# Kernel optimization log

Measured on AMD Instinct MI355X. Metric: run time of the kernel, lower is better.

The kernel has to match this reference:

```python
import jax, jax.numpy as jnp
import numpy as np
from jax import lax

B, S, E, H, V, L = 16, 256, 256, 256, 50000, 9


def setup_inputs() -> dict:
    key = jax.random.key(0)
    ks = jax.random.split(key, 12)
    s = 0.05
    return {
        "input_ids": jax.random.randint(ks[0], (B, S), 0, V),
        "attention_mask": jnp.ones((B, S), dtype=jnp.int32),
        "labels": jax.random.randint(ks[1], (B, S), 0, L),
        "embedding": jax.random.normal(ks[2], (V, E), jnp.float32) * s,
        "w_ih_l0": jax.random.normal(ks[3], (2, 4 * H, E), jnp.float32) * s,
        "w_ih_rest": jax.random.normal(ks[4], (3, 2, 4 * H, 2 * H), jnp.float32) * s,
        "w_hh": jax.random.normal(ks[5], (4, 2, 4 * H, H), jnp.float32) * s,
        "b": jax.random.normal(ks[6], (4, 2, 2, 4 * H), jnp.float32) * s,
        "ln_g": jnp.ones((2 * H,), jnp.float32),
        "ln_b": jnp.zeros((2 * H,), jnp.float32),
        "lin_w": jax.random.normal(ks[7], (L, 2 * H), jnp.float32) * s,
        "lin_b": jnp.zeros((L,), jnp.float32),
        "crf_start": jax.random.normal(ks[8], (L,), jnp.float32) * s,
        "crf_end": jax.random.normal(ks[9], (L,), jnp.float32) * s,
        "crf_trans": jax.random.normal(ks[10], (L, L), jnp.float32) * s,
    }


def _lstm_dir(x, w_ih, w_hh, b_ih, b_hh, reverse):
    # x: [B,S,in]; PyTorch gate order i,f,g,o packed along 4H.
    Bb = x.shape[0]
    Hh = w_hh.shape[1]
    xg = jnp.einsum('bsi,gi->bsg', x, w_ih) + b_ih + b_hh  # precompute input projection
    if reverse:
        xg = xg[:, ::-1]

    def step(carry, g):
        h, c = carry
        g = g + h @ w_hh.T
        i, f, gg, o = jnp.split(g, 4, axis=-1)
        c = jax.nn.sigmoid(f) * c + jax.nn.sigmoid(i) * jnp.tanh(gg)
        h = jax.nn.sigmoid(o) * jnp.tanh(c)
        return (h, c), h

    z = jnp.zeros((Bb, Hh), x.dtype)
    _, hs = lax.scan(step, (z, z), jnp.swapaxes(xg, 0, 1))
    hs = jnp.swapaxes(hs, 0, 1)  # [B,S,H]
    if reverse:
        hs = hs[:, ::-1]
    return hs


def _forward(input_ids, attention_mask, labels, embedding, w_ih_l0, w_ih_rest,
             w_hh, b, ln_g, ln_b, lin_w, lin_b, crf_start, crf_end, crf_trans):
    x = embedding[input_ids]  # [B,S,E]
    for layer in range(4):
        wf = w_ih_l0[0] if layer == 0 else w_ih_rest[layer - 1, 0]
        wb = w_ih_l0[1] if layer == 0 else w_ih_rest[layer - 1, 1]
        hf = _lstm_dir(x, wf, w_hh[layer, 0], b[layer, 0, 0], b[layer, 0, 1], False)
        hb = _lstm_dir(x, wb, w_hh[layer, 1], b[layer, 1, 0], b[layer, 1, 1], True)
        x = jnp.concatenate([hf, hb], axis=-1)  # [B,S,2H]
    # dropout is identity in eval mode
    mu = x.mean(-1, keepdims=True)
    var = ((x - mu) ** 2).mean(-1, keepdims=True)
    x = (x - mu) * lax.rsqrt(var + 1e-5) * ln_g + ln_b
    logits = jnp.einsum('bsh,lh->bsl', x, lin_w) + lin_b  # emissions [B,S,L]

    # CRF negative log-likelihood (torchcrf semantics, reduction='sum')
    Bb = logits.shape[0]
    mask_f = attention_mask.astype(logits.dtype)
    bidx = jnp.arange(Bb)
    first = labels[:, 0]
    num = crf_start[first] + logits[bidx, 0, first]
    em_t = jnp.swapaxes(logits, 0, 1)[1:]  # [S-1,B,L]
    tprev = labels[:, :-1].T
    tcur = labels[:, 1:].T
    mt = mask_f[:, 1:].T

    def num_step(s, inp):
        e, tp, tc, m = inp
        return s + (crf_trans[tp, tc] + e[bidx, tc]) * m, None

    num, _ = lax.scan(num_step, num, (em_t, tprev, tcur, mt))
    last = jnp.sum(attention_mask, axis=1).astype(jnp.int32) - 1
    num = num + crf_end[labels[bidx, last]]

    alpha = crf_start + logits[:, 0]  # [B,L]

    def den_step(a, inp):
        e, m = inp
        nxt = jax.nn.logsumexp(a[:, :, None] + crf_trans[None] + e[:, None, :], axis=1)
        return jnp.where(m[:, None] > 0, nxt, a), None

    alpha, _ = lax.scan(den_step, alpha, (em_t, mt))
    denom = jax.nn.logsumexp(alpha + crf_end, axis=-1)
    loss = -(num - denom).sum()
    return logits, loss


def reference(input_ids, attention_mask, labels, embedding, w_ih_l0, w_ih_rest,
              w_hh, b, ln_g, ln_b, lin_w, lin_b, crf_start, crf_end, crf_trans):
    return _forward(input_ids, attention_mask, labels, embedding, w_ih_l0,
                    w_ih_rest, w_hh, b, ln_g, ln_b, lin_w, lin_b,
                    crf_start, crf_end, crf_trans)
```

## Files before the change

### kernel.cpp

```cpp
#include <hip/hip_runtime.h>
#include <math.h>
#include <stdint.h>

#define BB 16
#define SS 256
#define LL 9
#define ROWS 4096
#define HP 272

typedef __attribute__((ext_vector_type(8))) short short8;
typedef __attribute__((ext_vector_type(4))) float f32x4;
typedef __attribute__((ext_vector_type(8))) int i32x8;

#define HSCALE 256.0f
#define LOG2E  1.44269504f
#define WCONST 1477.3199f
#define SCALE_ONE 0x7F7F7F7Fu
#define SCALE_IFO 0x6D6D6D6Du
#define SCALE_G   0x6E6E6E6Eu

__device__ __forceinline__ unsigned short f2bf(float f) {
  unsigned u = __float_as_uint(f);
  return (unsigned short)((u + 0x7FFF + ((u >> 16) & 1)) >> 16);
}
__device__ __forceinline__ float bf2f(unsigned short s) {
  return __uint_as_float(((unsigned)s) << 16);
}

__device__ __forceinline__ void gl2lds16(const void* g, void* l) {
  __builtin_amdgcn_global_load_lds(
      (const __attribute__((address_space(1))) void*)g,
      (__attribute__((address_space(3))) void*)l, 16, 0, 0);
}

__global__ __launch_bounds__(256) void embed_bf16(
    const int* __restrict__ ids, const float* __restrict__ emb,
    unsigned short* __restrict__ x0) {
  int row = blockIdx.x;
  int id = ids[row];
  x0[(size_t)row * 256 + threadIdx.x] = f2bf(emb[(size_t)id * 256 + threadIdx.x]);
}

__global__ __launch_bounds__(64) void pack_whh_mx(
    const float* __restrict__ w, unsigned* __restrict__ wfrag) {
  int nb = blockIdx.x, ks2 = blockIdx.y, z = blockIdx.z;
  int lane = threadIdx.x, qq = lane >> 4, col = lane & 15;
  int g = nb >> 4;
  float csc = (g == 2) ? WCONST : -WCONST;
  const float* wp = w + (size_t)z * 1024 * 256 + (size_t)(nb * 16 + col) * 256 +
                    ks2 * 128 + qq * 32;
  unsigned* op = wfrag + (((size_t)(z * 64 + nb) * 2 + ks2) * 64 + lane) * 8;
#pragma unroll
  for (int u = 0; u < 8; ++u) {
    float v0 = wp[u * 4 + 0] * csc, v1 = wp[u * 4 + 1] * csc;
    float v2 = wp[u * 4 + 2] * csc, v3 = wp[u * 4 + 3] * csc;
    unsigned pk = __builtin_amdgcn_cvt_pk_fp8_f32(v0, v1, 0, false);
    pk = __builtin_amdgcn_cvt_pk_fp8_f32(v2, v3, pk, true);
    op[u] = pk;
  }
}

__global__ __launch_bounds__(256) void bias_perm(
    const float* __restrict__ b2, float* __restrict__ biasPF) {
  int i = blockIdx.x * 256 + threadIdx.x;
  int l = i >> 11, r = i & 2047;
  int dir = r >> 10, np = r & 1023;
  int n = ((np & 3) << 8) + (np >> 2);
  float cg = ((np & 3) == 2) ? (2.0f * LOG2E) : (-LOG2E);
  biasPF[i] = (b2[l * 4096 + dir * 2048 + n] + b2[l * 4096 + dir * 2048 + 1024 + n]) * cg;
}

__global__ __launch_bounds__(256) void prep_wih(
    const float* __restrict__ w_l0, const float* __restrict__ w_rest,
    unsigned short* __restrict__ wp, const long* __restrict__ woff_dummy) {
  int l = blockIdx.z;
  int Ksh = l ? 9 : 8;
  int K = 1 << Ksh;
  long total = (long)2 * 1024 * K;
  long idx = (long)blockIdx.x * 256 + threadIdx.x;
  if (idx >= total) return;
  int k = (int)(idx & (K - 1));
  long r = idx >> Ksh;
  int np = (int)(r & 1023), dir = (int)(r >> 10);
  int nph = ((np & 3) << 8) + (np >> 2);
  float cg = ((np & 3) == 2) ? (2.0f * LOG2E) : (-LOG2E);
  const float* src = l ? (w_rest + (size_t)(l - 1) * 2 * 1024 * 512) : w_l0;
  size_t off = l ? (524288 + (size_t)(l - 1) * 1048576) : 0;
  wp[off + idx] = f2bf(src[((size_t)dir * 1024 + nph) * K + k] * cg);
}

__global__ __launch_bounds__(512) void gemm_xg128(
    const unsigned short* __restrict__ A, int K,
    const unsigned short* __restrict__ BP,
    const float* __restrict__ biasPF,
    unsigned short* __restrict__ xgP) {
  int dir = blockIdx.z;
  int n0 = blockIdx.x * 128, m0 = blockIdx.y * 128;
  int tid = threadIdx.x;
  int wv = tid >> 6, lane = tid & 63, quad = lane >> 4, col = lane & 15;
  __shared__ unsigned short As[128 * 32];
  __shared__ unsigned short Bs[128 * 32];
  const unsigned short* Bw = BP + (size_t)dir * 1024 * K;

  int srow = lane >> 2;
  int scol = (lane & 3) * 8;
  const unsigned short* ga = A + (size_t)(m0 + wv * 16 + srow) * K + scol;
  const unsigned short* gb = Bw + (size_t)(n0 + wv * 16 + srow) * K + scol;
  unsigned short* lA = &As[wv * 512];
  unsigned short* lB = &Bs[wv * 512];

  int wm = wv & 1;
  int wn = wv >> 1;
  f32x4 acc[4][2];
#pragma unroll
  for (int mt = 0; mt < 4; ++mt)
#pragma unroll
    for (int nt = 0; nt < 2; ++nt) acc[mt][nt] = (f32x4){0.f, 0.f, 0.f, 0.f};

  for (int k0 = 0; k0 < K; k0 += 32) {
    __syncthreads();
    gl2lds16(ga, lA);
    gl2lds16(gb, lB);
    ga += 32; gb += 32;
    __syncthreads();
    short8 bf0 = *(const short8*)&Bs[(wn * 32 + col) * 32 + quad * 8];
    short8 bf1 = *(const short8*)&Bs[(wn * 32 + 16 + col) * 32 + quad * 8];
#pragma unroll
    for (int mt = 0; mt < 4; ++mt) {
      short8 af = *(const short8*)&As[(wm * 64 + mt * 16 + col) * 32 + quad * 8];
      acc[mt][0] = __builtin_amdgcn_mfma_f32_16x16x32_bf16(af, bf0, acc[mt][0], 0, 0, 0);
      acc[mt][1] = __builtin_amdgcn_mfma_f32_16x16x32_bf16(af, bf1, acc[mt][1], 0, 0, 0);
    }
  }

#pragma unroll
  for (int nt = 0; nt < 2; ++nt) {
    int np = n0 + wn * 32 + nt * 16 + col;
    float bia = biasPF[dir * 1024 + np];
#pragma unroll
    for (int mt = 0; mt < 4; ++mt) {
#pragma unroll
      for (int r = 0; r < 4; ++r) {
        int row = m0 + wm * 64 + mt * 16 + quad * 4 + r;
        xgP[((size_t)dir * ROWS + row) * 1024 + np] = f2bf(acc[mt][nt][r] + bia);
      }
    }
  }
}

__global__ __launch_bounds__(512, 2) void lstm_mx(
    const unsigned short* __restrict__ xgP,
    const unsigned* __restrict__ wfrag,
    unsigned short* __restrict__ xout) {
  int dir = blockIdx.x & 1;
  int bg = blockIdx.x >> 1;
  int tid = threadIdx.x;
  int wv = tid >> 6, lane = tid & 63;
  int quad = lane >> 4, col = lane & 15;

  __shared__ __align__(16) unsigned char Hfrag[2][2 * HP];

  {
    int* hz = (int*)&Hfrag[0][0];
    for (int i = tid; i < HP; i += 512) hz[i] = 0;
  }

  i32x8 wf[2][4][2];
#pragma unroll
  for (int hbi = 0; hbi < 2; ++hbi)
#pragma unroll
    for (int g = 0; g < 4; ++g) {
      int nb = g * 16 + 2 * wv + hbi;
#pragma unroll
      for (int ks2 = 0; ks2 < 2; ++ks2)
        wf[hbi][g][ks2] = *(const i32x8*)(wfrag +
            (((size_t)(dir * 64 + nb) * 2 + ks2) * 64 + lane) * 8);
    }

  int aoff = ((lane & 15) >> 3) * HP + (lane >> 4) * 32;

  int hbsel = quad & 1;
  int bq = quad >> 1;
  int j = 32 * wv + 16 * hbsel + col;
  int b = bg * 2 + bq;
  int pos0 = dir ? (SS - 1) : 0;
  int dstep = dir ? -1 : 1;
  const unsigned short* xq_ptr =
      xgP + ((size_t)dir * ROWS + (size_t)b * SS + pos0) * 1024 + j * 4;
  unsigned short* xo_ptr = xout + ((size_t)b * SS + pos0) * 512 + dir * 256 + j;
  int xq_d = dstep * 1024;
  int xo_d = dstep * 512;
  int hw = bq * HP + j;

  float Cp = 0.f;
  unsigned short ph = 0;
  unsigned short* xo_prev = xo_ptr;
  int cur = 0;
  __syncthreads();

  for (int t = 0; t < SS; ++t) {
    if (t) *xo_prev = ph;
    ushort4 xq = *(const ushort4*)xq_ptr;
    xq_ptr += xq_d;

    i32x8 af0 = *(const i32x8*)&Hfrag[cur][aoff];
    i32x8 af1 = *(const i32x8*)&Hfrag[cur][aoff + 128];
    f32x4 acc[2][4];
#pragma unroll
    for (int hbi = 0; hbi < 2; ++hbi) {
#pragma unroll
      for (int g = 0; g < 4; ++g) {
        f32x4 a = (f32x4){0.f, 0.f, 0.f, 0.f};
        a = __builtin_amdgcn_mfma_scale_f32_16x16x128_f8f6f4(
                af0, wf[hbi][g][0], a, 0, 0, 0, SCALE_ONE, 0,
                (g == 2) ? SCALE_G : SCALE_IFO);
        a = __builtin_amdgcn_mfma_scale_f32_16x16x128_f8f6f4(
                af1, wf[hbi][g][1], a, 0, 0, 0, SCALE_ONE, 0,
                (g == 2) ? SCALE_G : SCALE_IFO);
        acc[hbi][g] = a;
      }
    }

    int nxt = cur ^ 1;
    float a_i = hbsel ? acc[1][0][0] : acc[0][0][0];
    float a_f = hbsel ? acc[1][1][0] : acc[0][1][0];
    float a_g = hbsel ? acc[1][2][0] : acc[0][2][0];
    float a_o = hbsel ? acc[1][3][0] : acc[0][3][0];
    float gi = a_i + bf2f(xq.x);
    float gf = a_f + bf2f(xq.y);
    float gt = a_g + bf2f(xq.z);
    float go = a_o + bf2f(xq.w);
    float si = __builtin_amdgcn_rcpf(1.0f + __builtin_amdgcn_exp2f(gi));
    float sf = __builtin_amdgcn_rcpf(1.0f + __builtin_amdgcn_exp2f(gf));
    float so = __builtin_amdgcn_rcpf(1.0f + __builtin_amdgcn_exp2f(go));
    float rg = __builtin_amdgcn_rcpf(1.0f + __builtin_amdgcn_exp2f(gt));
    float tg2 = fmaf(-4.0f * LOG2E, rg, 2.0f * LOG2E);
    Cp = fmaf(sf, Cp, si * tg2);
    float rc = __builtin_amdgcn_rcpf(1.0f + __builtin_amdgcn_exp2f(Cp));
    float h = so * fmaf(-2.0f, rc, 1.0f);
    unsigned pk = __builtin_amdgcn_cvt_pk_fp8_f32(h * HSCALE, h * HSCALE, 0, false);
    Hfrag[nxt][hw] = (unsigned char)(pk & 0xFF);
    ph = f2bf(h);
    xo_prev = xo_ptr;
    xo_ptr += xo_d;
    __syncthreads();
    cur = nxt;
  }
  *xo_prev = ph;
}

__global__ __launch_bounds__(64) void ln_logits(
    const unsigned short* __restrict__ X, const float* __restrict__ g,
    const float* __restrict__ bt, const float* __restrict__ W,
    const float* __restrict__ lb, float* __restrict__ out) {
  int row = blockIdx.x;
  int lane = threadIdx.x;
  const unsigned short* x = X + (size_t)row * 512;
  float v[8];
  float s = 0.f, s2 = 0.f;
#pragma unroll
  for (int i = 0; i < 8; ++i) {
    v[i] = bf2f(x[lane + 64 * i]);
    s += v[i];
    s2 += v[i] * v[i];
  }
#pragma unroll
  for (int off = 32; off; off >>= 1) {
    s += __shfl_down(s, off, 64);
    s2 += __shfl_down(s2, off, 64);
  }
  s = __shfl(s, 0, 64);
  s2 = __shfl(s2, 0, 64);
  float mu = s * (1.f / 512.f);
  float var = s2 * (1.f / 512.f) - mu * mu;
  float rstd = rsqrtf(var + 1e-5f);
  float y[8];
#pragma unroll
  for (int i = 0; i < 8; ++i) {
    int e = lane + 64 * i;
    y[i] = (v[i] - mu) * rstd * g[e] + bt[e];
  }
  for (int l = 0; l < LL; ++l) {
    float p = 0.f;
#pragma unroll
    for (int i = 0; i < 8; ++i) p += y[i] * W[(size_t)l * 512 + lane + 64 * i];
#pragma unroll
    for (int off = 32; off; off >>= 1) p += __shfl_down(p, off, 64);
    if (lane == 0) out[(size_t)row * LL + l] = p + lb[l];
  }
}

__global__ __launch_bounds__(256) void crf_kernel(
    const float* __restrict__ logits, const int* __restrict__ labels,
    const int* __restrict__ mask, const float* __restrict__ cs,
    const float* __restrict__ ce, const float* __restrict__ ct,
    float* __restrict__ loss_out) {
  __shared__ float trans[9][12];
  __shared__ float alpha[2][BB][12];
  __shared__ float numsh[BB];
  __shared__ float res[BB];
  int tid = threadIdx.x;
  int b = tid >> 4;
  int i = tid & 15;
  if (tid < 81) trans[tid / 9][tid % 9] = ct[tid];
  __syncthreads();
  const float* lg = logits + (size_t)b * SS * LL;
  const int* lbp = labels + (size_t)b * SS;
  const int* mk = mask + (size_t)b * SS;

  float np = 0.f;
  int msum = 0;
  for (int t = i; t < SS; t += 16) {
    msum += mk[t];
    if (t == 0) {
      int l0 = lbp[0];
      np += cs[l0] + lg[l0];
    } else {
      float m = (float)mk[t];
      np += (trans[lbp[t - 1]][lbp[t]] + lg[(size_t)t * LL + lbp[t]]) * m;
    }
  }
#pragma unroll
  for (int off = 8; off; off >>= 1) {
    np += __shfl_down(np, off, 16);
    msum += __shfl_down(msum, off, 16);
  }
  if (i == 0) {
    int last = msum - 1;
    numsh[b] = np + ce[lbp[last]];
  }

  if (i < LL) alpha[0][b][i] = cs[i] + lg[i];
  int cur = 0;
  for (int t = 1; t < SS; ++t) {
    if (i < LL) {
      float e = lg[(size_t)t * LL + i];
      float av[9];
      float mmax = -1e30f;
#pragma unroll
      for (int p = 0; p < LL; ++p) {
        float vv = alpha[cur][b][p] + trans[p][i];
        av[p] = vv;
        mmax = fmaxf(mmax, vv);
      }
      float ssum = 0.f;
#pragma unroll
      for (int p = 0; p < LL; ++p) ssum += __expf(av[p] - mmax);
      float anew = e + mmax + logf(ssum);
      float aold = alpha[cur][b][i];
      alpha[cur ^ 1][b][i] = (mk[t] > 0) ? anew : aold;
    }
    cur ^= 1;
  }
  if (i == 0) {
    float arr[9];
    float m2 = -1e30f;
#pragma unroll
    for (int cc = 0; cc < LL; ++cc) {
      arr[cc] = alpha[cur][b][cc] + ce[cc];
      m2 = fmaxf(m2, arr[cc]);
    }
    float ssd = 0.f;
#pragma unroll
    for (int cc = 0; cc < LL; ++cc) ssd += __expf(arr[cc] - m2);
    float denom = m2 + logf(ssd);
    res[b] = numsh[b] - denom;
  }
  __syncthreads();
  if (tid == 0) {
    float Lsum = 0.f;
    for (int b2 = 0; b2 < BB; ++b2) Lsum += res[b2];
    loss_out[0] = -Lsum;
  }
}

extern "C" void kernel_launch(void* const* d_in, const int* in_sizes, int n_in,
                              void* d_out, int out_size, void* d_ws, size_t ws_size,
                              hipStream_t stream) {
  const int* input_ids = (const int*)d_in[0];
  const int* attn_mask = (const int*)d_in[1];
  const int* labels = (const int*)d_in[2];
  const float* embedding = (const float*)d_in[3];
  const float* w_ih_l0 = (const float*)d_in[4];
  const float* w_ih_rest = (const float*)d_in[5];
  const float* w_hh = (const float*)d_in[6];
  const float* bvec = (const float*)d_in[7];
  const float* ln_g = (const float*)d_in[8];
  const float* ln_b = (const float*)d_in[9];
  const float* lin_w = (const float*)d_in[10];
  const float* lin_b = (const float*)d_in[11];
  const float* crf_start = (const float*)d_in[12];
  const float* crf_end = (const float*)d_in[13];
  const float* crf_trans = (const float*)d_in[14];
  float* out = (float*)d_out;
  char* base = (char*)d_ws;

  unsigned short* x0    = (unsigned short*)(base);
  unsigned short* xoutA = (unsigned short*)(base + (2u << 20));
  unsigned short* xoutB = (unsigned short*)(base + (6u << 20));
  unsigned short* xgP   = (unsigned short*)(base + (10u << 20));
  unsigned*       wfrag = (unsigned*)(base + (26u << 20));
  float*          biasPF= (float*)(base + (28u << 20));
  unsigned short* wihP  = (unsigned short*)(base + (29u << 20));

  embed_bf16<<<ROWS, 256, 0, stream>>>(input_ids, embedding, x0);
  pack_whh_mx<<<dim3(64, 2, 8), 64, 0, stream>>>(w_hh, wfrag);
  bias_perm<<<32, 256, 0, stream>>>(bvec, biasPF);
  prep_wih<<<dim3(4096, 1, 4), 256, 0, stream>>>(w_ih_l0, w_ih_rest, wihP, nullptr);

  const size_t WOFF[4] = {0, 524288, 1572864, 2621440};

  const unsigned short* cur = x0;
  unsigned short* nxt = xoutA;
  for (int l = 0; l < 4; ++l) {
    int K = l ? 512 : 256;
    gemm_xg128<<<dim3(8, 32, 2), 512, 0, stream>>>(
        cur, K, wihP + WOFF[l], biasPF + (size_t)l * 2048, xgP);
    lstm_mx<<<16, 512, 0, stream>>>(xgP, wfrag + (size_t)l * 131072, nxt);
    cur = nxt;
    nxt = (nxt == xoutA) ? xoutB : xoutA;
  }

  ln_logits<<<ROWS, 64, 0, stream>>>(cur, ln_g, ln_b, lin_w, lin_b, out);
  crf_kernel<<<1, 256, 0, stream>>>(out, labels, attn_mask, crf_start, crf_end,
                                    crf_trans, out + (size_t)ROWS * LL);
}
```

Measured before the change: 1.200 ms.

## Restructure LSTM recurrence to 1024-thread blocks covering four batch rows each

The recurrent kernel now runs 8 blocks of 16 waves, with each wave owning 16 hidden units across four batch rows, in place of 16 blocks of 8 waves handling two rows. Each wave now issues half as many MFMAs per step and holds half the weight fragments in registers. The input-projection gates are fed in as the MFMA accumulator seed and are prefetched one step ahead, and the bf16 output store is no longer deferred. The trade-off is that a barrier across 16 waves costs more per step, and fewer blocks mean fewer CUs are used.

```diff
diff --git a/kernel.cpp b/kernel.cpp
--- a/kernel.cpp
+++ b/kernel.cpp
@@ -148,7 +148,7 @@
   }
 }
 
-__global__ __launch_bounds__(512, 2) void lstm_mx(
+__global__ __launch_bounds__(1024, 4) void lstm_mx(
     const unsigned short* __restrict__ xgP,
     const unsigned* __restrict__ wfrag,
     unsigned short* __restrict__ xout) {
@@ -158,31 +158,27 @@
   int wv = tid >> 6, lane = tid & 63;
   int quad = lane >> 4, col = lane & 15;
 
-  __shared__ __align__(16) unsigned char Hfrag[2][2 * HP];
+  __shared__ __align__(16) unsigned char Hfrag[2][4 * HP];
 
   {
     int* hz = (int*)&Hfrag[0][0];
-    for (int i = tid; i < HP; i += 512) hz[i] = 0;
-  }
-
-  i32x8 wf[2][4][2];
-#pragma unroll
-  for (int hbi = 0; hbi < 2; ++hbi)
-#pragma unroll
-    for (int g = 0; g < 4; ++g) {
-      int nb = g * 16 + 2 * wv + hbi;
-#pragma unroll
-      for (int ks2 = 0; ks2 < 2; ++ks2)
-        wf[hbi][g][ks2] = *(const i32x8*)(wfrag +
-            (((size_t)(dir * 64 + nb) * 2 + ks2) * 64 + lane) * 8);
-    }
-
-  int aoff = ((lane & 15) >> 3) * HP + (lane >> 4) * 32;
-
-  int hbsel = quad & 1;
-  int bq = quad >> 1;
-  int j = 32 * wv + 16 * hbsel + col;
-  int b = bg * 2 + bq;
+    for (int i = tid; i < HP; i += 1024) hz[i] = 0;
+  }
+
+  i32x8 wf[4][2];
+#pragma unroll
+  for (int g = 0; g < 4; ++g) {
+    int nb = g * 16 + wv;
+#pragma unroll
+    for (int ks2 = 0; ks2 < 2; ++ks2)
+      wf[g][ks2] = *(const i32x8*)(wfrag +
+          (((size_t)(dir * 64 + nb) * 2 + ks2) * 64 + lane) * 8);
+  }
+
+  int aoff = ((lane & 15) >> 2) * HP + (lane >> 4) * 32;
+
+  int j = 16 * wv + col;
+  int b = bg * 4 + quad;
   int pos0 = dir ? (SS - 1) : 0;
   int dstep = dir ? -1 : 1;
   const unsigned short* xq_ptr =
@@ -190,46 +186,41 @@
   unsigned short* xo_ptr = xout + ((size_t)b * SS + pos0) * 512 + dir * 256 + j;
   int xq_d = dstep * 1024;
   int xo_d = dstep * 512;
-  int hw = bq * HP + j;
+  int hw = quad * HP + j;
 
   float Cp = 0.f;
-  unsigned short ph = 0;
-  unsigned short* xo_prev = xo_ptr;
   int cur = 0;
+  ushort4 xq_n = *(const ushort4*)xq_ptr;
+  xq_ptr += xq_d;
   __syncthreads();
 
   for (int t = 0; t < SS; ++t) {
-    if (t) *xo_prev = ph;
-    ushort4 xq = *(const ushort4*)xq_ptr;
+    ushort4 xq = xq_n;
+    xq_n = *(const ushort4*)xq_ptr;
     xq_ptr += xq_d;
 
     i32x8 af0 = *(const i32x8*)&Hfrag[cur][aoff];
     i32x8 af1 = *(const i32x8*)&Hfrag[cur][aoff + 128];
-    f32x4 acc[2][4];
-#pragma unroll
-    for (int hbi = 0; hbi < 2; ++hbi) {
-#pragma unroll
-      for (int g = 0; g < 4; ++g) {
-        f32x4 a = (f32x4){0.f, 0.f, 0.f, 0.f};
-        a = __builtin_amdgcn_mfma_scale_f32_16x16x128_f8f6f4(
-                af0, wf[hbi][g][0], a, 0, 0, 0, SCALE_ONE, 0,
-                (g == 2) ? SCALE_G : SCALE_IFO);
-        a = __builtin_amdgcn_mfma_scale_f32_16x16x128_f8f6f4(
-                af1, wf[hbi][g][1], a, 0, 0, 0, SCALE_ONE, 0,
-                (g == 2) ? SCALE_G : SCALE_IFO);
-        acc[hbi][g] = a;
-      }
+
+    f32x4 acc[4];
+    acc[0] = (f32x4){bf2f(xq.x), 0.f, 0.f, 0.f};
+    acc[1] = (f32x4){bf2f(xq.y), 0.f, 0.f, 0.f};
+    acc[2] = (f32x4){bf2f(xq.z), 0.f, 0.f, 0.f};
+    acc[3] = (f32x4){bf2f(xq.w), 0.f, 0.f, 0.f};
+#pragma unroll
+    for (int g = 0; g < 4; ++g) {
+      unsigned sb = (g == 2) ? SCALE_G : SCALE_IFO;
+      acc[g] = __builtin_amdgcn_mfma_scale_f32_16x16x128_f8f6f4(
+          af0, wf[g][0], acc[g], 0, 0, 0, SCALE_ONE, 0, sb);
+      acc[g] = __builtin_amdgcn_mfma_scale_f32_16x16x128_f8f6f4(
+          af1, wf[g][1], acc[g], 0, 0, 0, SCALE_ONE, 0, sb);
     }
 
     int nxt = cur ^ 1;
-    float a_i = hbsel ? acc[1][0][0] : acc[0][0][0];
-    float a_f = hbsel ? acc[1][1][0] : acc[0][1][0];
-    float a_g = hbsel ? acc[1][2][0] : acc[0][2][0];
-    float a_o = hbsel ? acc[1][3][0] : acc[0][3][0];
-    float gi = a_i + bf2f(xq.x);
-    float gf = a_f + bf2f(xq.y);
-    float gt = a_g + bf2f(xq.z);
-    float go = a_o + bf2f(xq.w);
+    float gi = acc[0][0];
+    float gf = acc[1][0];
+    float gt = acc[2][0];
+    float go = acc[3][0];
     float si = __builtin_amdgcn_rcpf(1.0f + __builtin_amdgcn_exp2f(gi));
     float sf = __builtin_amdgcn_rcpf(1.0f + __builtin_amdgcn_exp2f(gf));
     float so = __builtin_amdgcn_rcpf(1.0f + __builtin_amdgcn_exp2f(go));
@@ -240,13 +231,11 @@
     float h = so * fmaf(-2.0f, rc, 1.0f);
     unsigned pk = __builtin_amdgcn_cvt_pk_fp8_f32(h * HSCALE, h * HSCALE, 0, false);
     Hfrag[nxt][hw] = (unsigned char)(pk & 0xFF);
-    ph = f2bf(h);
-    xo_prev = xo_ptr;
+    *xo_ptr = f2bf(h);
     xo_ptr += xo_d;
     __syncthreads();
     cur = nxt;
   }
-  *xo_prev = ph;
 }
 
 __global__ __launch_bounds__(64) void ln_logits(
@@ -416,7 +405,7 @@
     int K = l ? 512 : 256;
     gemm_xg128<<<dim3(8, 32, 2), 512, 0, stream>>>(
         cur, K, wihP + WOFF[l], biasPF + (size_t)l * 2048, xgP);
-    lstm_mx<<<16, 512, 0, stream>>>(xgP, wfrag + (size_t)l * 131072, nxt);
+    lstm_mx<<<8, 1024, 0, stream>>>(xgP, wfrag + (size_t)l * 131072, nxt);
     cur = nxt;
     nxt = (nxt == xoutA) ? xoutB : xoutA;
   }
```

Result: faster. 1.004 ms (-16.3%).
